# Optimization experiments

Measured on AMD Instinct MI355X. Metric: run time of the kernel, lower is better.

The kernel has to match this reference:

```python
import jax, jax.numpy as jnp
import numpy as np

NUM_GROUPS = 8
EPS = 1e-6

def group_norm(x, gamma, beta):
    # x: [B, C, L]
    B, C, L = x.shape
    g = x.reshape(B, NUM_GROUPS, (C // NUM_GROUPS) * L)
    mean = g.mean(axis=-1, keepdims=True)
    var = g.var(axis=-1, keepdims=True)
    g = (g - mean) * jax.lax.rsqrt(var + EPS)
    g = g.reshape(B, C, L)
    return g * gamma[None, :, None] + beta[None, :, None]

def conv1x1(h, w, b):
    # w: [O, C], b: [O]; h: [B, C, L]
    return jnp.einsum('oc,bcl->bol', w, h) + b[None, :, None]

def setup_inputs() -> dict:
    key = jax.random.key(0)
    ks = jax.random.split(key, 12)
    B, C, L = 8, 512, 2048
    s = 1.0 / np.sqrt(C)
    inp = {
        'x': jax.random.normal(ks[0], (B, C, L), dtype=jnp.float32),
        'gamma': jnp.ones((C,), jnp.float32),
        'beta': jnp.zeros((C,), jnp.float32),
        'wq': jax.random.uniform(ks[1], (C, C), jnp.float32, -s, s),
        'bq': jax.random.uniform(ks[2], (C,), jnp.float32, -s, s),
        'wk': jax.random.uniform(ks[3], (C, C), jnp.float32, -s, s),
        'bk': jax.random.uniform(ks[4], (C,), jnp.float32, -s, s),
        'wv': jax.random.uniform(ks[5], (C, C), jnp.float32, -s, s),
        'bv': jax.random.uniform(ks[6], (C,), jnp.float32, -s, s),
        'wo': jax.random.uniform(ks[7], (C, C), jnp.float32, -s, s),
        'bo': jax.random.uniform(ks[8], (C,), jnp.float32, -s, s),
    }
    return inp

def reference(x, gamma, beta, wq, bq, wk, bk, wv, bv, wo, bo):
    C = x.shape[1]
    h = group_norm(x, gamma, beta)
    q = conv1x1(h, wq, bq)  # [B, C, L]
    k = conv1x1(h, wk, bk)
    v = conv1x1(h, wv, bv)
    # scores: [B, Lq, Lk] = q^T k, scaled by C^-0.5
    w = jnp.einsum('bci,bcj->bij', q, k) * (C ** -0.5)
    w = jax.nn.softmax(w, axis=2)
    # h[b,c,i] = sum_j v[b,c,j] * w[b,i,j]
    h = jnp.einsum('bcj,bij->bci', v, w)
    h = conv1x1(h, wo, bo)
    return x + h
```

## Files before the change

kernel.cpp:

```cpp
#include <hip/hip_runtime.h>
#include <hip/hip_bf16.h>
#include <cstdio>

typedef __attribute__((ext_vector_type(8))) short short8;
typedef __attribute__((ext_vector_type(8))) unsigned short ushort8;
typedef __attribute__((ext_vector_type(4))) float f32x4;
typedef __attribute__((ext_vector_type(4))) unsigned short ushort4v;

__device__ inline unsigned short f2bf(float f){
    unsigned int u = __float_as_uint(f);
    unsigned int r = (u + 0x7fffu + ((u >> 16) & 1u)) >> 16;
    return (unsigned short)r;
}
__device__ inline float bf2f(unsigned short b){
    return __uint_as_float((unsigned int)b << 16);
}

template<bool NT> __device__ inline void store1(float* p, float v){
    if (NT) __builtin_nontemporal_store(v, p); else *p = v;
}
template<bool NT> __device__ inline void store1(unsigned short* p, float v){
    unsigned short b = f2bf(v);
    if (NT) __builtin_nontemporal_store(b, p); else *p = b;
}

#define BM 128
#define BN 128

template<typename OutT, int EPI, bool NTST>
__global__ __launch_bounds__(256)
void gemm_nt(const unsigned short* __restrict__ Ag,
             const unsigned short* __restrict__ Bg,
             OutT* __restrict__ Cg,
             int K, int lda, int ldb, int ldc,
             long sA, long sB, long sC,
             const float* __restrict__ bias,
             const float* __restrict__ resid, long sR,
             float scale)
{
    const int gx = gridDim.x, gy = gridDim.y;
    const int nwg  = gx * gy * (int)gridDim.z;
    const int orig = blockIdx.x + gx * (blockIdx.y + gy * blockIdx.z);
    const int cpx  = nwg >> 3;
    const int nid  = (orig & 7) * cpx + (orig >> 3);
    const int bx   = nid % gx;
    const int tmp  = nid / gx;
    const int by   = tmp % gy;
    const int bz   = tmp / gy;

    Ag += (long)bz * sA;
    Bg += (long)bz * sB;
    Cg += (long)bz * sC;
    const int m0 = by * BM;
    const int n0 = bx * BN;

    __shared__ unsigned short As[128 * 64];
    __shared__ unsigned short Bs[128 * 64];

    const int t    = threadIdx.x;
    const int wave = t >> 6;
    const int lane = t & 63;
    const int wm   = (wave >> 1) << 6;
    const int wn   = (wave & 1) << 6;
    const int lhi  = lane >> 4;
    const int llo  = lane & 15;

    f32x4 acc[4][4];
#pragma unroll
    for (int i = 0; i < 4; i++)
#pragma unroll
        for (int j = 0; j < 4; j++) acc[i][j] = (f32x4)(0.0f);

    for (int k0 = 0; k0 < K; k0 += 64){
        __syncthreads();
#pragma unroll
        for (int i = 0; i < 4; i++){
            const int tt = i * 256 + t;
            const int r  = tt >> 3;
            const int cb = tt & 7;
            const int cs = cb ^ (r & 7);
            const unsigned short* gpA = Ag + (long)(m0 + r) * lda + k0 + cs * 8;
            const unsigned short* gpB = Bg + (long)(n0 + r) * ldb + k0 + cs * 8;
            unsigned short* lpA = As + i * 2048 + wave * 512;
            unsigned short* lpB = Bs + i * 2048 + wave * 512;
            __builtin_amdgcn_global_load_lds(
                (const __attribute__((address_space(1))) void*)gpA,
                (__attribute__((address_space(3))) void*)lpA, 16, 0, 0);
            __builtin_amdgcn_global_load_lds(
                (const __attribute__((address_space(1))) void*)gpB,
                (__attribute__((address_space(3))) void*)lpB, 16, 0, 0);
        }
        __syncthreads();

#pragma unroll
        for (int ksub = 0; ksub < 2; ksub++){
            short8 af[4], bf[4];
#pragma unroll
            for (int mi = 0; mi < 4; mi++){
                const int r  = wm + mi * 16 + llo;
                const int cs = (ksub * 4 + lhi) ^ (r & 7);
                af[mi] = *(const short8*)(As + r * 64 + cs * 8);
            }
#pragma unroll
            for (int ni = 0; ni < 4; ni++){
                const int r  = wn + ni * 16 + llo;
                const int cs = (ksub * 4 + lhi) ^ (r & 7);
                bf[ni] = *(const short8*)(Bs + r * 64 + cs * 8);
            }
#pragma unroll
            for (int mi = 0; mi < 4; mi++)
#pragma unroll
                for (int ni = 0; ni < 4; ni++)
                    acc[mi][ni] = __builtin_amdgcn_mfma_f32_16x16x32_bf16(
                        af[mi], bf[ni], acc[mi][ni], 0, 0, 0);
        }
    }

#pragma unroll
    for (int mi = 0; mi < 4; mi++){
#pragma unroll
        for (int ni = 0; ni < 4; ni++){
            const int n  = n0 + wn + ni * 16 + llo;
            const int mb = m0 + wm + mi * 16 + lhi * 4;
            f32x4 v = acc[mi][ni];
#pragma unroll
            for (int j = 0; j < 4; j++){
                const int m = mb + j;
                float val = v[j] * scale;
                if (EPI == 1) val += bias[n];
                if (EPI == 2) val += bias[m];
                if (EPI == 3) val += bias[m] + resid[(long)bz * sR + (long)m * ldc + n];
                store1<NTST>(&Cg[(long)m * ldc + n], val);
            }
        }
    }
}


__global__ void gn_partial(const float* __restrict__ x, float* __restrict__ part){
    const long base = (long)blockIdx.x * 8192;
    const float4* xp = (const float4*)(x + base);
    float s = 0.f, ss = 0.f;
    for (int i = threadIdx.x; i < 2048; i += 256){
        float4 v = xp[i];
        s  += (v.x + v.y) + (v.z + v.w);
        ss += (v.x * v.x + v.y * v.y) + (v.z * v.z + v.w * v.w);
    }
    for (int o = 32; o; o >>= 1){ s += __shfl_down(s, o); ss += __shfl_down(ss, o); }
    __shared__ float rs[4], rss[4];
    const int wave = threadIdx.x >> 6, lane = threadIdx.x & 63;
    if (lane == 0){ rs[wave] = s; rss[wave] = ss; }
    __syncthreads();
    if (threadIdx.x == 0){
        part[blockIdx.x * 2]     = (rs[0] + rs[1]) + (rs[2] + rs[3]);
        part[blockIdx.x * 2 + 1] = (rss[0] + rss[1]) + (rss[2] + rss[3]);
    }
}

__global__ void gn_final(const float* __restrict__ part, float* __restrict__ stats){
    const int bg = threadIdx.x;
    if (bg >= 64) return;
    float s = 0.f, ss = 0.f;
    for (int c = 0; c < 16; c++){
        s  += part[(bg * 16 + c) * 2];
        ss += part[(bg * 16 + c) * 2 + 1];
    }
    const float inv_n = 1.0f / 131072.0f;
    const float mean = s * inv_n;
    const float var  = ss * inv_n - mean * mean;
    stats[bg * 2]     = mean;
    stats[bg * 2 + 1] = rsqrtf(var + 1e-6f);
}

__global__ void norm_transpose(const float* __restrict__ x, const float* __restrict__ stats,
                               const float* __restrict__ gamma, const float* __restrict__ beta,
                               unsigned short* __restrict__ ht){
    const int b = blockIdx.z, c0 = blockIdx.y * 64, l0 = blockIdx.x * 64;
    const int bg = b * 8 + (c0 >> 6);
    const float mean = stats[bg * 2], rstd = stats[bg * 2 + 1];
    __shared__ unsigned short tile[64][66];
    const float* xb = x + (long)b * 1048576;
    const int t = threadIdx.x;
#pragma unroll
    for (int i = 0; i < 16; i++){
        const int idx = i * 256 + t;
        const int c = idx >> 6, l = idx & 63;
        float v = xb[(long)(c0 + c) * 2048 + l0 + l];
        v = (v - mean) * rstd * gamma[c0 + c] + beta[c0 + c];
        tile[l][c] = f2bf(v);
    }
    __syncthreads();
    unsigned short* htb = ht + (long)b * 1048576;
#pragma unroll
    for (int i = 0; i < 16; i++){
        const int idx = i * 256 + t;
        const int l = idx >> 6, c = idx & 63;
        htb[(long)(l0 + l) * 512 + c0 + c] = tile[l][c];
    }
}

__global__ void f32_to_bf16(const float4* __restrict__ in, ushort4v* __restrict__ out, int n4){
    const int i = blockIdx.x * 256 + threadIdx.x;
    if (i >= n4) return;
    float4 v = in[i];
    ushort4v o;
    o.x = f2bf(v.x); o.y = f2bf(v.y); o.z = f2bf(v.z); o.w = f2bf(v.w);
    out[i] = o;
}

__global__ void softmax_inplace(unsigned short* __restrict__ p){
    const long base = (long)blockIdx.x * 2048;
    ushort8* pp = (ushort8*)(p + base);
    const int t = threadIdx.x;
    ushort8 v = pp[t];
    float f[8];
#pragma unroll
    for (int j = 0; j < 8; j++) f[j] = bf2f(v[j]);
    float mx = f[0];
#pragma unroll
    for (int j = 1; j < 8; j++) mx = fmaxf(mx, f[j]);
    for (int o = 32; o; o >>= 1) mx = fmaxf(mx, __shfl_xor(mx, o));
    __shared__ float rmax[4], rsum[4];
    const int wave = t >> 6, lane = t & 63;
    if (lane == 0) rmax[wave] = mx;
    __syncthreads();
    mx = fmaxf(fmaxf(rmax[0], rmax[1]), fmaxf(rmax[2], rmax[3]));
    float sum = 0.f;
#pragma unroll
    for (int j = 0; j < 8; j++){ f[j] = __expf(f[j] - mx); sum += f[j]; }
    for (int o = 32; o; o >>= 1) sum += __shfl_xor(sum, o);
    if (lane == 0) rsum[wave] = sum;
    __syncthreads();
    sum = (rsum[0] + rsum[1]) + (rsum[2] + rsum[3]);
    const float inv = 1.0f / sum;
    ushort8 o8;
#pragma unroll
    for (int j = 0; j < 8; j++) o8[j] = f2bf(f[j] * inv);
    pp[t] = o8;
}

enum : long {
    OFF_WQ  = 0,
    OFF_WK  = 524288,
    OFF_WV  = 1048576,
    OFF_WO  = 1572864,
    OFF_HT  = 2097152,
    OFF_QT  = OFF_HT  + 16777216,
    OFF_KT  = OFF_QT  + 16777216,
    OFF_V   = OFF_KT  + 16777216,
    OFF_H2  = OFF_V   + 16777216,
    OFF_P   = OFF_H2  + 16777216,
    OFF_GNP = OFF_P   + 67108864,
    OFF_GNS = OFF_GNP + 8192,
    OFF_END = OFF_GNS + 512
};

extern "C" void kernel_launch(void* const* d_in, const int* in_sizes, int n_in,
                              void* d_out, int out_size, void* d_ws, size_t ws_size,
                              hipStream_t stream)
{
    const float* x     = (const float*)d_in[0];
    const float* gamma = (const float*)d_in[1];
    const float* beta  = (const float*)d_in[2];
    const float* wq    = (const float*)d_in[3];
    const float* bq    = (const float*)d_in[4];
    const float* wk    = (const float*)d_in[5];
    const float* bk    = (const float*)d_in[6];
    const float* wv    = (const float*)d_in[7];
    const float* bv    = (const float*)d_in[8];
    const float* wo    = (const float*)d_in[9];
    const float* bo    = (const float*)d_in[10];
    float* out = (float*)d_out;
    char* ws = (char*)d_ws;

    if (ws_size < (size_t)OFF_END){
        fprintf(stderr, "kernel_launch: ws too small (%zu < %ld)\n", ws_size, (long)OFF_END);
        return;
    }

    unsigned short* WQb = (unsigned short*)(ws + OFF_WQ);
    unsigned short* WKb = (unsigned short*)(ws + OFF_WK);
    unsigned short* WVb = (unsigned short*)(ws + OFF_WV);
    unsigned short* WOb = (unsigned short*)(ws + OFF_WO);
    unsigned short* HT  = (unsigned short*)(ws + OFF_HT);
    unsigned short* QT  = (unsigned short*)(ws + OFF_QT);
    unsigned short* KT  = (unsigned short*)(ws + OFF_KT);
    unsigned short* V   = (unsigned short*)(ws + OFF_V);
    unsigned short* H2  = (unsigned short*)(ws + OFF_H2);
    unsigned short* P   = (unsigned short*)(ws + OFF_P);
    float*          GNP = (float*)(ws + OFF_GNP);
    float*          GNS = (float*)(ws + OFF_GNS);

    const long LC = 1048576;
    const long LL = 4194304;

    f32_to_bf16<<<256, 256, 0, stream>>>((const float4*)wq, (ushort4v*)WQb, 65536);
    f32_to_bf16<<<256, 256, 0, stream>>>((const float4*)wk, (ushort4v*)WKb, 65536);
    f32_to_bf16<<<256, 256, 0, stream>>>((const float4*)wv, (ushort4v*)WVb, 65536);
    f32_to_bf16<<<256, 256, 0, stream>>>((const float4*)wo, (ushort4v*)WOb, 65536);

    gn_partial<<<1024, 256, 0, stream>>>(x, GNP);
    gn_final<<<1, 64, 0, stream>>>(GNP, GNS);
    norm_transpose<<<dim3(32, 8, 8), 256, 0, stream>>>(x, GNS, gamma, beta, HT);

    gemm_nt<unsigned short, 1, false><<<dim3(4, 16, 8), 256, 0, stream>>>(
        HT, WQb, QT, 512, 512, 512, 512, LC, 0, LC, bq, nullptr, 0, 1.0f);
    gemm_nt<unsigned short, 1, false><<<dim3(4, 16, 8), 256, 0, stream>>>(
        HT, WKb, KT, 512, 512, 512, 512, LC, 0, LC, bk, nullptr, 0, 1.0f);
    gemm_nt<unsigned short, 2, false><<<dim3(16, 4, 8), 256, 0, stream>>>(
        WVb, HT, V, 512, 512, 512, 2048, 0, LC, LC, bv, nullptr, 0, 1.0f);

    gemm_nt<unsigned short, 0, true><<<dim3(16, 16, 8), 256, 0, stream>>>(
        QT, KT, P, 512, 512, 512, 2048, LC, LC, LL, nullptr, nullptr, 0, 0.04419417382f);

    softmax_inplace<<<16384, 256, 0, stream>>>(P);

    gemm_nt<unsigned short, 0, false><<<dim3(4, 16, 8), 256, 0, stream>>>(
        P, V, H2, 2048, 2048, 2048, 512, LL, LC, LC, nullptr, nullptr, 0, 1.0f);

    gemm_nt<float, 3, false><<<dim3(16, 4, 8), 256, 0, stream>>>(
        WOb, H2, out, 512, 512, 512, 2048, 0, LC, LC, bo, x, LC, 1.0f);
}
```

Baseline: 309.9 us.

## Double-buffer LDS tiles in the GEMM and merge weight conversion launches

The bf16 GEMM now keeps two LDS buffers for A and B. It issues the global-to-LDS loads for the next K tile before running the MFMAs on the current tile, with one barrier per iteration instead of two, so load latency can overlap compute. The four weight-conversion launches become one kernel that writes into a contiguous workspace region starting at OFF_WQ, which assumes the four weight buffers sit back to back. The nontemporal-store template option is removed, so the score matrix P is now written with normal stores. LDS per block doubles to 64 KB, which may limit how many blocks fit on a CU.

```diff
diff --git a/kernel.cpp b/kernel.cpp
--- a/kernel.cpp
+++ b/kernel.cpp
@@ -16,18 +16,13 @@
     return __uint_as_float((unsigned int)b << 16);
 }
 
-template<bool NT> __device__ inline void store1(float* p, float v){
-    if (NT) __builtin_nontemporal_store(v, p); else *p = v;
-}
-template<bool NT> __device__ inline void store1(unsigned short* p, float v){
-    unsigned short b = f2bf(v);
-    if (NT) __builtin_nontemporal_store(b, p); else *p = b;
-}
+__device__ inline void store1(float* p, float v){ *p = v; }
+__device__ inline void store1(unsigned short* p, float v){ *p = f2bf(v); }
 
 #define BM 128
 #define BN 128
 
-template<typename OutT, int EPI, bool NTST>
+template<typename OutT, int EPI>
 __global__ __launch_bounds__(256)
 void gemm_nt(const unsigned short* __restrict__ Ag,
              const unsigned short* __restrict__ Bg,
@@ -54,8 +49,8 @@
     const int m0 = by * BM;
     const int n0 = bx * BN;
 
-    __shared__ unsigned short As[128 * 64];
-    __shared__ unsigned short Bs[128 * 64];
+    __shared__ unsigned short As[2][128 * 64];
+    __shared__ unsigned short Bs[2][128 * 64];
 
     const int t    = threadIdx.x;
     const int wave = t >> 6;
@@ -71,8 +66,7 @@
 #pragma unroll
         for (int j = 0; j < 4; j++) acc[i][j] = (f32x4)(0.0f);
 
-    for (int k0 = 0; k0 < K; k0 += 64){
-        __syncthreads();
+    auto stage = [&](int bi, int k0){
 #pragma unroll
         for (int i = 0; i < 4; i++){
             const int tt = i * 256 + t;
@@ -81,8 +75,8 @@
             const int cs = cb ^ (r & 7);
             const unsigned short* gpA = Ag + (long)(m0 + r) * lda + k0 + cs * 8;
             const unsigned short* gpB = Bg + (long)(n0 + r) * ldb + k0 + cs * 8;
-            unsigned short* lpA = As + i * 2048 + wave * 512;
-            unsigned short* lpB = Bs + i * 2048 + wave * 512;
+            unsigned short* lpA = &As[bi][i * 2048 + wave * 512];
+            unsigned short* lpB = &Bs[bi][i * 2048 + wave * 512];
             __builtin_amdgcn_global_load_lds(
                 (const __attribute__((address_space(1))) void*)gpA,
                 (__attribute__((address_space(3))) void*)lpA, 16, 0, 0);
@@ -90,8 +84,15 @@
                 (const __attribute__((address_space(1))) void*)gpB,
                 (__attribute__((address_space(3))) void*)lpB, 16, 0, 0);
         }
-        __syncthreads();
-
+    };
+
+    const int nt = K >> 6;
+    stage(0, 0);
+    __syncthreads();
+
+    int cur = 0;
+    for (int kt = 0; kt < nt; kt++){
+        if (kt + 1 < nt) stage(cur ^ 1, (kt + 1) << 6);
 #pragma unroll
         for (int ksub = 0; ksub < 2; ksub++){
             short8 af[4], bf[4];
@@ -99,13 +100,13 @@
             for (int mi = 0; mi < 4; mi++){
                 const int r  = wm + mi * 16 + llo;
                 const int cs = (ksub * 4 + lhi) ^ (r & 7);
-                af[mi] = *(const short8*)(As + r * 64 + cs * 8);
+                af[mi] = *(const short8*)(&As[cur][r * 64 + cs * 8]);
             }
 #pragma unroll
             for (int ni = 0; ni < 4; ni++){
                 const int r  = wn + ni * 16 + llo;
                 const int cs = (ksub * 4 + lhi) ^ (r & 7);
-                bf[ni] = *(const short8*)(Bs + r * 64 + cs * 8);
+                bf[ni] = *(const short8*)(&Bs[cur][r * 64 + cs * 8]);
             }
 #pragma unroll
             for (int mi = 0; mi < 4; mi++)
@@ -114,6 +115,8 @@
                     acc[mi][ni] = __builtin_amdgcn_mfma_f32_16x16x32_bf16(
                         af[mi], bf[ni], acc[mi][ni], 0, 0, 0);
         }
+        __syncthreads();
+        cur ^= 1;
     }
 
 #pragma unroll
@@ -130,7 +133,7 @@
                 if (EPI == 1) val += bias[n];
                 if (EPI == 2) val += bias[m];
                 if (EPI == 3) val += bias[m] + resid[(long)bz * sR + (long)m * ldc + n];
-                store1<NTST>(&Cg[(long)m * ldc + n], val);
+                store1(&Cg[(long)m * ldc + n], val);
             }
         }
     }
@@ -199,10 +202,13 @@
     }
 }
 
-__global__ void f32_to_bf16(const float4* __restrict__ in, ushort4v* __restrict__ out, int n4){
+__global__ void weights_to_bf16(const float4* __restrict__ wq, const float4* __restrict__ wk,
+                                const float4* __restrict__ wv, const float4* __restrict__ wo,
+                                ushort4v* __restrict__ out){
     const int i = blockIdx.x * 256 + threadIdx.x;
-    if (i >= n4) return;
-    float4 v = in[i];
+    const int w = i >> 16, off = i & 65535;
+    const float4* src = (w == 0) ? wq : (w == 1) ? wk : (w == 2) ? wv : wo;
+    float4 v = src[off];
     ushort4v o;
     o.x = f2bf(v.x); o.y = f2bf(v.y); o.z = f2bf(v.z); o.w = f2bf(v.w);
     out[i] = o;
@@ -278,10 +284,6 @@
         return;
     }
 
-    unsigned short* WQb = (unsigned short*)(ws + OFF_WQ);
-    unsigned short* WKb = (unsigned short*)(ws + OFF_WK);
-    unsigned short* WVb = (unsigned short*)(ws + OFF_WV);
-    unsigned short* WOb = (unsigned short*)(ws + OFF_WO);
     unsigned short* HT  = (unsigned short*)(ws + OFF_HT);
     unsigned short* QT  = (unsigned short*)(ws + OFF_QT);
     unsigned short* KT  = (unsigned short*)(ws + OFF_KT);
@@ -290,34 +292,37 @@
     unsigned short* P   = (unsigned short*)(ws + OFF_P);
     float*          GNP = (float*)(ws + OFF_GNP);
     float*          GNS = (float*)(ws + OFF_GNS);
+    unsigned short* WQb = (unsigned short*)(ws + OFF_WQ);
+    unsigned short* WKb = (unsigned short*)(ws + OFF_WK);
+    unsigned short* WVb = (unsigned short*)(ws + OFF_WV);
+    unsigned short* WOb = (unsigned short*)(ws + OFF_WO);
 
     const long LC = 1048576;
     const long LL = 4194304;
 
-    f32_to_bf16<<<256, 256, 0, stream>>>((const float4*)wq, (ushort4v*)WQb, 65536);
-    f32_to_bf16<<<256, 256, 0, stream>>>((const float4*)wk, (ushort4v*)WKb, 65536);
-    f32_to_bf16<<<256, 256, 0, stream>>>((const float4*)wv, (ushort4v*)WVb, 65536);
-    f32_to_bf16<<<256, 256, 0, stream>>>((const float4*)wo, (ushort4v*)WOb, 65536);
+    weights_to_bf16<<<1024, 256, 0, stream>>>(
+        (const float4*)wq, (const float4*)wk, (const float4*)wv, (const float4*)wo,
+        (ushort4v*)(ws + OFF_WQ));
 
     gn_partial<<<1024, 256, 0, stream>>>(x, GNP);
     gn_final<<<1, 64, 0, stream>>>(GNP, GNS);
     norm_transpose<<<dim3(32, 8, 8), 256, 0, stream>>>(x, GNS, gamma, beta, HT);
 
-    gemm_nt<unsigned short, 1, false><<<dim3(4, 16, 8), 256, 0, stream>>>(
+    gemm_nt<unsigned short, 1><<<dim3(4, 16, 8), 256, 0, stream>>>(
         HT, WQb, QT, 512, 512, 512, 512, LC, 0, LC, bq, nullptr, 0, 1.0f);
-    gemm_nt<unsigned short, 1, false><<<dim3(4, 16, 8), 256, 0, stream>>>(
+    gemm_nt<unsigned short, 1><<<dim3(4, 16, 8), 256, 0, stream>>>(
         HT, WKb, KT, 512, 512, 512, 512, LC, 0, LC, bk, nullptr, 0, 1.0f);
-    gemm_nt<unsigned short, 2, false><<<dim3(16, 4, 8), 256, 0, stream>>>(
+    gemm_nt<unsigned short, 2><<<dim3(16, 4, 8), 256, 0, stream>>>(
         WVb, HT, V, 512, 512, 512, 2048, 0, LC, LC, bv, nullptr, 0, 1.0f);
 
-    gemm_nt<unsigned short, 0, true><<<dim3(16, 16, 8), 256, 0, stream>>>(
+    gemm_nt<unsigned short, 0><<<dim3(16, 16, 8), 256, 0, stream>>>(
         QT, KT, P, 512, 512, 512, 2048, LC, LC, LL, nullptr, nullptr, 0, 0.04419417382f);
 
     softmax_inplace<<<16384, 256, 0, stream>>>(P);
 
-    gemm_nt<unsigned short, 0, false><<<dim3(4, 16, 8), 256, 0, stream>>>(
+    gemm_nt<unsigned short, 0><<<dim3(4, 16, 8), 256, 0, stream>>>(
         P, V, H2, 2048, 2048, 2048, 512, LL, LC, LC, nullptr, nullptr, 0, 1.0f);
 
-    gemm_nt<float, 3, false><<<dim3(16, 4, 8), 256, 0, stream>>>(
+    gemm_nt<float, 3><<<dim3(16, 4, 8), 256, 0, stream>>>(
         WOb, H2, out, 512, 512, 512, 2048, 0, LC, LC, bo, x, LC, 1.0f);
 }
```

Measured after the change: 285.8 us. -7.8%, faster.
